# Kernel tuning notes

Measured on AMD Instinct MI355X. Metric: run time of the kernel, lower is better.

## Reference

```python
import jax, jax.numpy as jnp
import numpy as np

B, T, H = 16, 2048, 1024
L_ORDER, R_ORDER = 1, 1
K = L_ORDER + R_ORDER + 1
THRESH = 1.0


def _alphas(hidden, conv_w, conv_b, lin_w, lin_b):
    # hidden: [B, T, H]
    context = jnp.swapaxes(hidden, 1, 2)  # [B, H, T]
    q = jnp.pad(context, ((0, 0), (0, 0), (L_ORDER, R_ORDER)))  # ConstantPad1d
    mem = jax.lax.conv_general_dilated(
        q, conv_w, (1,), 'VALID',
        dimension_numbers=('NCH', 'OIH', 'NCH'),
        feature_group_count=conv_w.shape[0])  # depthwise conv, groups=idim
    mem = mem + conv_b[None, :, None]
    out = jnp.swapaxes(mem + context, 1, 2)  # [B, T, H] (dropout = identity, eval)
    out = jax.nn.relu(out)
    out = out @ lin_w.T + lin_b  # [B, T, 1]
    return jax.nn.sigmoid(out)[..., 0]  # [B, T]


def _cif_scan(hidden, alphas, threshold):
    # sequential integrate-and-fire over time, vectorized over batch via lax.scan
    b, t, h = hidden.shape

    def step(carry, xs):
        integrate, frame = carry          # [B], [B, H]
        alpha, h_t = xs                   # [B], [B, H]
        dist = 1.0 - integrate            # distribution_completion
        integrate = integrate + alpha
        fires_t = integrate
        fire = integrate >= threshold
        integrate = jnp.where(fire, integrate - 1.0, integrate)
        cur = jnp.where(fire, dist, alpha)
        rem = alpha - cur
        frame = frame + cur[:, None] * h_t
        frames_t = frame
        frame = jnp.where(fire[:, None], rem[:, None] * h_t, frame)
        return (integrate, frame), (fires_t, frames_t)

    init = (jnp.zeros((b,), hidden.dtype), jnp.zeros((b, h), hidden.dtype))
    xs = (jnp.swapaxes(alphas, 0, 1), jnp.swapaxes(hidden, 0, 1))
    _, (fires, frames) = jax.lax.scan(step, init, xs)
    return jnp.swapaxes(frames, 0, 1), jnp.swapaxes(fires, 0, 1)  # [B,T,H], [B,T]


def _gather_fired(frames, fires, threshold, max_label_len):
    # per-batch select frames where fires>=threshold, pad to max_label_len
    b, t, h = frames.shape
    mask = fires >= threshold                         # [B, T]
    rank = jnp.cumsum(mask.astype(jnp.int32), axis=1) - 1
    idx = jnp.where(mask, rank, max_label_len)        # invalid -> dummy row
    out = jnp.zeros((b, max_label_len + 1, h), frames.dtype)
    out = out.at[jnp.arange(b)[:, None], idx].add(
        jnp.where(mask[..., None], frames, 0.0))
    return out[:, :max_label_len]


def setup_inputs() -> dict:
    key = jax.random.key(0)
    k1, k2, k3, k4 = jax.random.split(key, 4)
    hidden = jax.random.normal(k1, (B, T, H), jnp.float32)
    conv_w = jax.random.normal(k2, (H, 1, K), jnp.float32) / np.sqrt(K)
    conv_b = jax.random.normal(k3, (H,), jnp.float32) * 0.01
    lin_w = jax.random.normal(k4, (1, H), jnp.float32) / np.sqrt(H)
    lin_b = jnp.zeros((1,), jnp.float32)
    return {"hidden": hidden, "conv_w": conv_w, "conv_b": conv_b,
            "lin_w": lin_w, "lin_b": lin_b}


def reference(hidden, conv_w, conv_b, lin_w, lin_b):
    alphas = _alphas(hidden, conv_w, conv_b, lin_w, lin_b)  # [B, T]
    cif_length = alphas.sum(-1)                             # [B]
    frames, fires = _cif_scan(hidden, alphas, THRESH)
    # data-dependent output length (matches torch: round(alphas.sum(-1)).max())
    max_label_len = int(jnp.round(cif_length).astype(jnp.int32).max())
    cif_output = _gather_fired(frames, fires, THRESH, max_label_len)
    return cif_output, cif_length, fires
```

## Files before the change

kernel.cpp:

```cpp
#include <hip/hip_runtime.h>
#include <math.h>

#define B_ 16
#define T_ 2048
#define H_ 1024
#define TPB 16
#define KPB 8

__global__ __launch_bounds__(256) void k1_alphas(
    const float* __restrict__ hidden, const float* __restrict__ conv_w,
    const float* __restrict__ conv_b, const float* __restrict__ lin_w,
    const float* __restrict__ lin_b, float* __restrict__ alphas)
{
    const int tile = blockIdx.x & (T_ / TPB - 1);
    const int b    = blockIdx.x / (T_ / TPB);
    const int tid  = threadIdx.x;
    const int h0   = tid * 4;

    float w0[4], w1[4], w2[4];
    {
        const float4* cw = (const float4*)(conv_w + (size_t)h0 * 3);
        float4 c0 = cw[0], c1 = cw[1], c2 = cw[2];
        w0[0] = c0.x; w1[0] = c0.y; w2[0] = c0.z;
        w0[1] = c0.w; w1[1] = c1.x; w2[1] = c1.y;
        w0[2] = c1.z; w1[2] = c1.w; w2[2] = c2.x;
        w0[3] = c2.y; w1[3] = c2.z; w2[3] = c2.w;
    }
    const float4 cb = *(const float4*)(conv_b + h0);
    const float4 lw = *(const float4*)(lin_w + h0);
    const float  lb = lin_b[0];

    const size_t base = ((size_t)b * T_) * H_ + h0;
    const int t0 = tile * TPB;

    float4 prev = (t0 > 0) ? *(const float4*)(hidden + base + (size_t)(t0 - 1) * H_)
                           : make_float4(0.f, 0.f, 0.f, 0.f);
    float4 curr = *(const float4*)(hidden + base + (size_t)t0 * H_);
    float4 next;

    __shared__ float lds[4][TPB];
    const int wave = tid >> 6;
    const int lane = tid & 63;

    #pragma unroll
    for (int tt = 0; tt < TPB; ++tt) {
        const int t = t0 + tt;
        next = (t + 1 < T_) ? *(const float4*)(hidden + base + (size_t)(t + 1) * H_)
                            : make_float4(0.f, 0.f, 0.f, 0.f);
        float p = 0.f, v;
        v = fmaf(w0[0], prev.x, fmaf(w1[0], curr.x, fmaf(w2[0], next.x, cb.x + curr.x)));
        p = fmaf(fmaxf(v, 0.f), lw.x, p);
        v = fmaf(w0[1], prev.y, fmaf(w1[1], curr.y, fmaf(w2[1], next.y, cb.y + curr.y)));
        p = fmaf(fmaxf(v, 0.f), lw.y, p);
        v = fmaf(w0[2], prev.z, fmaf(w1[2], curr.z, fmaf(w2[2], next.z, cb.z + curr.z)));
        p = fmaf(fmaxf(v, 0.f), lw.z, p);
        v = fmaf(w0[3], prev.w, fmaf(w1[3], curr.w, fmaf(w2[3], next.w, cb.w + curr.w)));
        p = fmaf(fmaxf(v, 0.f), lw.w, p);
        #pragma unroll
        for (int m = 32; m; m >>= 1) p += __shfl_xor(p, m);
        if (lane == 0) lds[wave][tt] = p;
        prev = curr; curr = next;
    }
    __syncthreads();
    if (tid < TPB) {
        float s = lds[0][tid] + lds[1][tid] + lds[2][tid] + lds[3][tid] + lb;
        alphas[(size_t)b * T_ + t0 + tid] = 1.f / (1.f + expf(-s));
    }
}

__global__ __launch_bounds__(256) void k2_scan_coef(
    const float* __restrict__ alphas, float* __restrict__ fires,
    float* __restrict__ wgt,
    int* __restrict__ fire_pos, int* __restrict__ n_fires,
    float* __restrict__ cif_length, int Lpad)
{
    const int b = blockIdx.x;
    const int tid = threadIdx.x;
    const size_t base = (size_t)b * T_;

    __shared__ float sA[T_];
    __shared__ float sF[T_];

    {
        const int i = tid * 8;
        *(float4*)(sA + i)     = *(const float4*)(alphas + base + i);
        *(float4*)(sA + i + 4) = *(const float4*)(alphas + base + i + 4);
    }
    __syncthreads();

    if (tid == 0) {
        float I = 0.f;
        for (int t = 0; t < T_; t += 8) {
            #pragma unroll
            for (int j = 0; j < 8; ++j) {
                I += sA[t + j];
                sF[t + j] = I;
                I = __builtin_amdgcn_fractf(I);
            }
        }
    }
    __syncthreads();

    const int t0 = tid * 8;
    float a[8], f[8];
    #pragma unroll
    for (int j = 0; j < 8; ++j) { a[j] = sA[t0 + j]; f[j] = sF[t0 + j]; }
    const float fprev = (t0 == 0) ? 0.f : sF[t0 - 1];

    *(float4*)(fires + base + t0)     = make_float4(f[0], f[1], f[2], f[3]);
    *(float4*)(fires + base + t0 + 4) = make_float4(f[4], f[5], f[6], f[7]);

    float w[16];
    bool fr[8];
    float asum = 0.f;
    int cnt = 0;
    #pragma unroll
    for (int j = 0; j < 8; ++j) {
        float fp = (j == 0) ? fprev : f[j - 1];
        float Iprev = __builtin_amdgcn_fractf(fp);
        fr[j] = (f[j] >= 1.f);
        const float dist = 1.f - Iprev;
        const float cu = fr[j] ? dist : a[j];
        const float re = a[j] - cu;
        w[2 * j]     = cu;
        w[2 * j + 1] = fr[j] ? re : -1.f;
        cnt += fr[j] ? 1 : 0;
        asum += a[j];
    }
    {
        const size_t wb = ((size_t)b * T_ + t0) * 2;
        *(float4*)(wgt + wb)      = *(float4*)(w);
        *(float4*)(wgt + wb + 4)  = *(float4*)(w + 4);
        *(float4*)(wgt + wb + 8)  = *(float4*)(w + 8);
        *(float4*)(wgt + wb + 12) = *(float4*)(w + 12);
    }

    const int lane = tid & 63, wave = tid >> 6;
    int inc = cnt;
    #pragma unroll
    for (int d = 1; d < 64; d <<= 1) {
        int v = __shfl_up(inc, d);
        if (lane >= d) inc += v;
    }
    __shared__ int wsum[4];
    if (lane == 63) wsum[wave] = inc;
    __syncthreads();
    int waveoff = 0;
    for (int w2 = 0; w2 < wave; ++w2) waveoff += wsum[w2];
    int r = waveoff + inc - cnt;
    #pragma unroll
    for (int j = 0; j < 8; ++j) {
        if (fr[j]) {
            if (r < Lpad) fire_pos[b * Lpad + r] = t0 + j;
            ++r;
        }
    }
    if (tid == 255) n_fires[b] = waveoff + inc;

    float s = asum;
    #pragma unroll
    for (int m = 32; m; m >>= 1) s += __shfl_xor(s, m);
    __shared__ float wred[4];
    if (lane == 0) wred[wave] = s;
    __syncthreads();
    if (tid == 0) cif_length[b] = wred[0] + wred[1] + wred[2] + wred[3];
}

__global__ __launch_bounds__(256) void k3_frames(
    const float* __restrict__ hidden, const float* __restrict__ wgt,
    const int* __restrict__ fire_pos, const int* __restrict__ n_fires,
    float* __restrict__ out, int L, int Lpad)
{
    const int k0 = blockIdx.x * KPB;
    const int b  = blockIdx.y;
    const int tid = threadIdx.x;
    const int h0 = tid * 4;
    const size_t hb = ((size_t)b * T_) * H_ + h0;
    const float2* wb = (const float2*)wgt + (size_t)b * T_;

    const int n = __builtin_amdgcn_readfirstlane(n_fires[b]);
    const int kmax = min(KPB, L - k0);
    const int kact = min(kmax, n - k0);

    const float4 zero4 = make_float4(0.f, 0.f, 0.f, 0.f);
    if (kact <= 0) {
        for (int kk = 0; kk < kmax; ++kk)
            *(float4*)(out + ((size_t)b * L + (k0 + kk)) * H_ + h0) = zero4;
        return;
    }

    const int tend = __builtin_amdgcn_readfirstlane(fire_pos[b * Lpad + k0 + kact - 1]);

    float4 acc;
    int t;
    if (k0 > 0) {
        const int s0 = __builtin_amdgcn_readfirstlane(fire_pos[b * Lpad + k0 - 1]);
        const float4 hr = *(const float4*)(hidden + hb + (size_t)s0 * H_);
        const float rm = wb[s0].y;
        acc.x = rm * hr.x; acc.y = rm * hr.y; acc.z = rm * hr.z; acc.w = rm * hr.w;
        t = s0 + 1;
    } else {
        acc = zero4;
        t = 0;
    }

    float4 hA, hB, hC;
    float2 wA, wB, wC;
    hA = *(const float4*)(hidden + hb + (size_t)t * H_);
    wA = wb[t];
    if (t + 1 <= tend) {
        hB = *(const float4*)(hidden + hb + (size_t)(t + 1) * H_);
        wB = wb[t + 1];
    } else { hB = zero4; wB = make_float2(0.f, -1.f); }

    int kk = 0;
    while (t <= tend) {
        if (t + 2 <= tend) {
            hC = *(const float4*)(hidden + hb + (size_t)(t + 2) * H_);
            wC = wb[t + 2];
        } else { hC = zero4; wC = make_float2(0.f, -1.f); }

        acc.x = fmaf(wA.x, hA.x, acc.x);
        acc.y = fmaf(wA.x, hA.y, acc.y);
        acc.z = fmaf(wA.x, hA.z, acc.z);
        acc.w = fmaf(wA.x, hA.w, acc.w);
        if (wA.y >= 0.f) {
            *(float4*)(out + ((size_t)b * L + (k0 + kk)) * H_ + h0) = acc;
            acc.x = wA.y * hA.x; acc.y = wA.y * hA.y;
            acc.z = wA.y * hA.z; acc.w = wA.y * hA.w;
            ++kk;
        }
        hA = hB; wA = wB; hB = hC; wB = wC;
        ++t;
    }

    for (; kk < kmax; ++kk)
        *(float4*)(out + ((size_t)b * L + (k0 + kk)) * H_ + h0) = zero4;
}

extern "C" void kernel_launch(void* const* d_in, const int* in_sizes, int n_in,
                              void* d_out, int out_size, void* d_ws, size_t ws_size,
                              hipStream_t stream) {
    const float* hidden = (const float*)d_in[0];
    const float* conv_w = (const float*)d_in[1];
    const float* conv_b = (const float*)d_in[2];
    const float* lin_w  = (const float*)d_in[3];
    const float* lin_b  = (const float*)d_in[4];
    float* out = (float*)d_out;

    const int L = (out_size - B_ - B_ * T_) / (B_ * H_);
    float* cif_output = out;
    float* cif_length = out + (size_t)B_ * L * H_;
    float* fires      = cif_length + B_;

    float* alphas = (float*)d_ws;
    float* wgt    = alphas + (size_t)B_ * T_;
    const int Lpad = L + 8;
    int* fire_pos = (int*)(wgt + (size_t)2 * B_ * T_);
    int* n_fires  = fire_pos + (size_t)B_ * Lpad;

    k1_alphas<<<dim3(B_ * (T_ / TPB)), 256, 0, stream>>>(
        hidden, conv_w, conv_b, lin_w, lin_b, alphas);
    k2_scan_coef<<<dim3(B_), 256, 0, stream>>>(
        alphas, fires, wgt, fire_pos, n_fires, cif_length, Lpad);
    k3_frames<<<dim3((L + KPB - 1) / KPB, B_), 256, 0, stream>>>(
        hidden, wgt, fire_pos, n_fires, cif_output, L, Lpad);
}
```

Measured before the change: 261.8 us.

## Fuse three CIF kernels into one persistent kernel with atomic work queues

Replaces the three separate launches (alphas, scan/coefficients, frame gather) with a single persistent kernel of fixed grid size. Blocks pull work items from atomic counters and use per-batch completion flags with acquire/release spinning, so a batch's scan and gather can start as soon as its alphas are done instead of waiting for the whole previous kernel. This removes launch gaps and lets the stages overlap across batches. In exchange it adds a memset, atomics, spin-waits and the risk of deadlock if the grid is not fully co-resident.

```diff
diff --git a/kernel.cpp b/kernel.cpp
--- a/kernel.cpp
+++ b/kernel.cpp
@@ -6,236 +6,294 @@
 #define H_ 1024
 #define TPB 16
 #define KPB 8
-
-__global__ __launch_bounds__(256) void k1_alphas(
+#define NK1 (B_ * (T_ / TPB))
+#define GRID 1024
+
+struct Flags {
+    int qK1, qK2, qK3, pad;
+    int k1_done[B_];
+    int k2_done[B_];
+};
+
+__device__ __forceinline__ int acq_load(int* p) {
+    return __hip_atomic_load(p, __ATOMIC_ACQUIRE, __HIP_MEMORY_SCOPE_AGENT);
+}
+
+union ShMem {
+    float k1lds[4][TPB];
+    struct { float sA[T_]; float sF[T_]; } k2;
+};
+
+__global__ __launch_bounds__(256, 4) void cif_fused(
     const float* __restrict__ hidden, const float* __restrict__ conv_w,
     const float* __restrict__ conv_b, const float* __restrict__ lin_w,
-    const float* __restrict__ lin_b, float* __restrict__ alphas)
+    const float* __restrict__ lin_b,
+    float* __restrict__ alphas, float* __restrict__ wgt,
+    int* __restrict__ fire_pos, int* __restrict__ n_fires,
+    Flags* flags,
+    float* __restrict__ out, float* __restrict__ cif_length,
+    float* __restrict__ fires, int L, int Lpad, int cpb, int totK3)
 {
-    const int tile = blockIdx.x & (T_ / TPB - 1);
-    const int b    = blockIdx.x / (T_ / TPB);
+    __shared__ ShMem sh;
+    __shared__ int sh_item;
+    __shared__ int wsum[4];
+    __shared__ float wred[4];
+
     const int tid  = threadIdx.x;
-    const int h0   = tid * 4;
-
-    float w0[4], w1[4], w2[4];
+    const int lane = tid & 63;
+    const int wave = tid >> 6;
+
     {
-        const float4* cw = (const float4*)(conv_w + (size_t)h0 * 3);
-        float4 c0 = cw[0], c1 = cw[1], c2 = cw[2];
-        w0[0] = c0.x; w1[0] = c0.y; w2[0] = c0.z;
-        w0[1] = c0.w; w1[1] = c1.x; w2[1] = c1.y;
-        w0[2] = c1.z; w1[2] = c1.w; w2[2] = c2.x;
-        w0[3] = c2.y; w1[3] = c2.z; w2[3] = c2.w;
+        const int h0 = tid * 4;
+        float w0[4], w1[4], w2[4];
+        {
+            const float4* cw = (const float4*)(conv_w + (size_t)h0 * 3);
+            float4 c0 = cw[0], c1 = cw[1], c2 = cw[2];
+            w0[0] = c0.x; w1[0] = c0.y; w2[0] = c0.z;
+            w0[1] = c0.w; w1[1] = c1.x; w2[1] = c1.y;
+            w0[2] = c1.z; w1[2] = c1.w; w2[2] = c2.x;
+            w0[3] = c2.y; w1[3] = c2.z; w2[3] = c2.w;
+        }
+        const float4 cb = *(const float4*)(conv_b + h0);
+        const float4 lw = *(const float4*)(lin_w + h0);
+        const float  lb = lin_b[0];
+
+        for (;;) {
+            if (tid == 0) sh_item = atomicAdd(&flags->qK1, 1);
+            __syncthreads();
+            const int it = sh_item;
+            if (it >= NK1) break;
+
+            const int b    = it >> 7;
+            const int tile = it & 127;
+            const size_t base = ((size_t)b * T_) * H_ + h0;
+            const int t0 = tile * TPB;
+
+            float4 prev = (t0 > 0) ? *(const float4*)(hidden + base + (size_t)(t0 - 1) * H_)
+                                   : make_float4(0.f, 0.f, 0.f, 0.f);
+            float4 curr = *(const float4*)(hidden + base + (size_t)t0 * H_);
+            float4 next;
+
+            #pragma unroll
+            for (int tt = 0; tt < TPB; ++tt) {
+                const int t = t0 + tt;
+                next = (t + 1 < T_) ? *(const float4*)(hidden + base + (size_t)(t + 1) * H_)
+                                    : make_float4(0.f, 0.f, 0.f, 0.f);
+                float p = 0.f, v;
+                v = fmaf(w0[0], prev.x, fmaf(w1[0], curr.x, fmaf(w2[0], next.x, cb.x + curr.x)));
+                p = fmaf(fmaxf(v, 0.f), lw.x, p);
+                v = fmaf(w0[1], prev.y, fmaf(w1[1], curr.y, fmaf(w2[1], next.y, cb.y + curr.y)));
+                p = fmaf(fmaxf(v, 0.f), lw.y, p);
+                v = fmaf(w0[2], prev.z, fmaf(w1[2], curr.z, fmaf(w2[2], next.z, cb.z + curr.z)));
+                p = fmaf(fmaxf(v, 0.f), lw.z, p);
+                v = fmaf(w0[3], prev.w, fmaf(w1[3], curr.w, fmaf(w2[3], next.w, cb.w + curr.w)));
+                p = fmaf(fmaxf(v, 0.f), lw.w, p);
+                #pragma unroll
+                for (int m = 32; m; m >>= 1) p += __shfl_xor(p, m);
+                if (lane == 0) sh.k1lds[wave][tt] = p;
+                prev = curr; curr = next;
+            }
+            __syncthreads();
+            if (tid < TPB) {
+                float s = sh.k1lds[0][tid] + sh.k1lds[1][tid] + sh.k1lds[2][tid]
+                        + sh.k1lds[3][tid] + lb;
+                alphas[(size_t)b * T_ + t0 + tid] = 1.f / (1.f + expf(-s));
+            }
+            if (tid == 0) {
+                __threadfence();
+                atomicAdd(&flags->k1_done[b], 1);
+            }
+            __syncthreads();
+        }
     }
-    const float4 cb = *(const float4*)(conv_b + h0);
-    const float4 lw = *(const float4*)(lin_w + h0);
-    const float  lb = lin_b[0];
-
-    const size_t base = ((size_t)b * T_) * H_ + h0;
-    const int t0 = tile * TPB;
-
-    float4 prev = (t0 > 0) ? *(const float4*)(hidden + base + (size_t)(t0 - 1) * H_)
-                           : make_float4(0.f, 0.f, 0.f, 0.f);
-    float4 curr = *(const float4*)(hidden + base + (size_t)t0 * H_);
-    float4 next;
-
-    __shared__ float lds[4][TPB];
-    const int wave = tid >> 6;
-    const int lane = tid & 63;
-
-    #pragma unroll
-    for (int tt = 0; tt < TPB; ++tt) {
-        const int t = t0 + tt;
-        next = (t + 1 < T_) ? *(const float4*)(hidden + base + (size_t)(t + 1) * H_)
-                            : make_float4(0.f, 0.f, 0.f, 0.f);
-        float p = 0.f, v;
-        v = fmaf(w0[0], prev.x, fmaf(w1[0], curr.x, fmaf(w2[0], next.x, cb.x + curr.x)));
-        p = fmaf(fmaxf(v, 0.f), lw.x, p);
-        v = fmaf(w0[1], prev.y, fmaf(w1[1], curr.y, fmaf(w2[1], next.y, cb.y + curr.y)));
-        p = fmaf(fmaxf(v, 0.f), lw.y, p);
-        v = fmaf(w0[2], prev.z, fmaf(w1[2], curr.z, fmaf(w2[2], next.z, cb.z + curr.z)));
-        p = fmaf(fmaxf(v, 0.f), lw.z, p);
-        v = fmaf(w0[3], prev.w, fmaf(w1[3], curr.w, fmaf(w2[3], next.w, cb.w + curr.w)));
-        p = fmaf(fmaxf(v, 0.f), lw.w, p);
-        #pragma unroll
-        for (int m = 32; m; m >>= 1) p += __shfl_xor(p, m);
-        if (lane == 0) lds[wave][tt] = p;
-        prev = curr; curr = next;
+
+    for (;;) {
+        if (tid == 0) sh_item = atomicAdd(&flags->qK2, 1);
+        __syncthreads();
+        const int b = sh_item;
+        if (b >= B_) break;
+
+        if (tid == 0) {
+            while (acq_load(&flags->k1_done[b]) < (T_ / TPB))
+                __builtin_amdgcn_s_sleep(8);
+        }
+        __syncthreads();
+        __threadfence();
+
+        const size_t base = (size_t)b * T_;
+        {
+            const int i = tid * 8;
+            *(float4*)(sh.k2.sA + i)     = *(const float4*)(alphas + base + i);
+            *(float4*)(sh.k2.sA + i + 4) = *(const float4*)(alphas + base + i + 4);
+        }
+        __syncthreads();
+
+        if (tid == 0) {
+            float I = 0.f;
+            for (int t = 0; t < T_; t += 8) {
+                #pragma unroll
+                for (int j = 0; j < 8; ++j) {
+                    I += sh.k2.sA[t + j];
+                    sh.k2.sF[t + j] = I;
+                    I = __builtin_amdgcn_fractf(I);
+                }
+            }
+        }
+        __syncthreads();
+
+        const int t0 = tid * 8;
+        float a[8], f[8];
+        #pragma unroll
+        for (int j = 0; j < 8; ++j) { a[j] = sh.k2.sA[t0 + j]; f[j] = sh.k2.sF[t0 + j]; }
+        const float fprev = (t0 == 0) ? 0.f : sh.k2.sF[t0 - 1];
+
+        *(float4*)(fires + base + t0)     = make_float4(f[0], f[1], f[2], f[3]);
+        *(float4*)(fires + base + t0 + 4) = make_float4(f[4], f[5], f[6], f[7]);
+
+        float w[16];
+        bool fr[8];
+        float asum = 0.f;
+        int cnt = 0;
+        #pragma unroll
+        for (int j = 0; j < 8; ++j) {
+            float fp = (j == 0) ? fprev : f[j - 1];
+            float Iprev = __builtin_amdgcn_fractf(fp);
+            fr[j] = (f[j] >= 1.f);
+            const float dist = 1.f - Iprev;
+            const float cu = fr[j] ? dist : a[j];
+            const float re = a[j] - cu;
+            w[2 * j]     = cu;
+            w[2 * j + 1] = fr[j] ? re : -1.f;
+            cnt += fr[j] ? 1 : 0;
+            asum += a[j];
+        }
+        {
+            const size_t wb = ((size_t)b * T_ + t0) * 2;
+            *(float4*)(wgt + wb)      = *(float4*)(w);
+            *(float4*)(wgt + wb + 4)  = *(float4*)(w + 4);
+            *(float4*)(wgt + wb + 8)  = *(float4*)(w + 8);
+            *(float4*)(wgt + wb + 12) = *(float4*)(w + 12);
+        }
+
+        int inc = cnt;
+        #pragma unroll
+        for (int d = 1; d < 64; d <<= 1) {
+            int v = __shfl_up(inc, d);
+            if (lane >= d) inc += v;
+        }
+        if (lane == 63) wsum[wave] = inc;
+        __syncthreads();
+        int waveoff = 0;
+        for (int w2 = 0; w2 < wave; ++w2) waveoff += wsum[w2];
+        int r = waveoff + inc - cnt;
+        #pragma unroll
+        for (int j = 0; j < 8; ++j) {
+            if (fr[j]) {
+                if (r < Lpad) fire_pos[b * Lpad + r] = t0 + j;
+                ++r;
+            }
+        }
+        if (tid == 255) n_fires[b] = waveoff + inc;
+
+        float s = asum;
+        #pragma unroll
+        for (int m = 32; m; m >>= 1) s += __shfl_xor(s, m);
+        if (lane == 0) wred[wave] = s;
+        __syncthreads();
+        if (tid == 0) {
+            cif_length[b] = wred[0] + wred[1] + wred[2] + wred[3];
+            __threadfence();
+            __hip_atomic_store(&flags->k2_done[b], 1, __ATOMIC_RELEASE,
+                               __HIP_MEMORY_SCOPE_AGENT);
+        }
+        __syncthreads();
     }
-    __syncthreads();
-    if (tid < TPB) {
-        float s = lds[0][tid] + lds[1][tid] + lds[2][tid] + lds[3][tid] + lb;
-        alphas[(size_t)b * T_ + t0 + tid] = 1.f / (1.f + expf(-s));
+
+    {
+        const int h0 = tid * 4;
+        int last_b = -1;
+        for (;;) {
+            if (tid == 0) sh_item = atomicAdd(&flags->qK3, 1);
+            __syncthreads();
+            const int j = sh_item;
+            if (j >= totK3) break;
+            const int b  = j / cpb;
+            const int k0 = (j - b * cpb) * KPB;
+
+            if (b != last_b) {
+                if (tid == 0) {
+                    while (acq_load(&flags->k2_done[b]) == 0)
+                        __builtin_amdgcn_s_sleep(32);
+                }
+                __syncthreads();
+                __threadfence();
+                last_b = b;
+            }
+
+            const size_t hb = ((size_t)b * T_) * H_ + h0;
+            const float2* wb = (const float2*)wgt + (size_t)b * T_;
+            const int n = __builtin_amdgcn_readfirstlane(n_fires[b]);
+            const int kmax = min(KPB, L - k0);
+            const int kact = min(kmax, n - k0);
+            const float4 zero4 = make_float4(0.f, 0.f, 0.f, 0.f);
+
+            if (kact <= 0) {
+                for (int kk = 0; kk < kmax; ++kk)
+                    *(float4*)(out + ((size_t)b * L + (k0 + kk)) * H_ + h0) = zero4;
+            } else {
+                const int tend = __builtin_amdgcn_readfirstlane(
+                    fire_pos[b * Lpad + k0 + kact - 1]);
+
+                float4 acc;
+                int t;
+                if (k0 > 0) {
+                    const int s0 = __builtin_amdgcn_readfirstlane(
+                        fire_pos[b * Lpad + k0 - 1]);
+                    const float4 hr = *(const float4*)(hidden + hb + (size_t)s0 * H_);
+                    const float rm = wb[s0].y;
+                    acc.x = rm * hr.x; acc.y = rm * hr.y;
+                    acc.z = rm * hr.z; acc.w = rm * hr.w;
+                    t = s0 + 1;
+                } else {
+                    acc = zero4;
+                    t = 0;
+                }
+
+                float4 hA, hB, hC;
+                float2 wA, wB, wC;
+                hA = *(const float4*)(hidden + hb + (size_t)t * H_);
+                wA = wb[t];
+                if (t + 1 <= tend) {
+                    hB = *(const float4*)(hidden + hb + (size_t)(t + 1) * H_);
+                    wB = wb[t + 1];
+                } else { hB = zero4; wB = make_float2(0.f, -1.f); }
+
+                int kk = 0;
+                while (t <= tend) {
+                    if (t + 2 <= tend) {
+                        hC = *(const float4*)(hidden + hb + (size_t)(t + 2) * H_);
+                        wC = wb[t + 2];
+                    } else { hC = zero4; wC = make_float2(0.f, -1.f); }
+
+                    acc.x = fmaf(wA.x, hA.x, acc.x);
+                    acc.y = fmaf(wA.x, hA.y, acc.y);
+                    acc.z = fmaf(wA.x, hA.z, acc.z);
+                    acc.w = fmaf(wA.x, hA.w, acc.w);
+                    if (wA.y >= 0.f) {
+                        *(float4*)(out + ((size_t)b * L + (k0 + kk)) * H_ + h0) = acc;
+                        acc.x = wA.y * hA.x; acc.y = wA.y * hA.y;
+                        acc.z = wA.y * hA.z; acc.w = wA.y * hA.w;
+                        ++kk;
+                    }
+                    hA = hB; wA = wB; hB = hC; wB = wC;
+                    ++t;
+                }
+                for (; kk < kmax; ++kk)
+                    *(float4*)(out + ((size_t)b * L + (k0 + kk)) * H_ + h0) = zero4;
+            }
+            __syncthreads();
+        }
     }
-}
-
-__global__ __launch_bounds__(256) void k2_scan_coef(
-    const float* __restrict__ alphas, float* __restrict__ fires,
-    float* __restrict__ wgt,
-    int* __restrict__ fire_pos, int* __restrict__ n_fires,
-    float* __restrict__ cif_length, int Lpad)
-{
-    const int b = blockIdx.x;
-    const int tid = threadIdx.x;
-    const size_t base = (size_t)b * T_;
-
-    __shared__ float sA[T_];
-    __shared__ float sF[T_];
-
-    {
-        const int i = tid * 8;
-        *(float4*)(sA + i)     = *(const float4*)(alphas + base + i);
-        *(float4*)(sA + i + 4) = *(const float4*)(alphas + base + i + 4);
-    }
-    __syncthreads();
-
-    if (tid == 0) {
-        float I = 0.f;
-        for (int t = 0; t < T_; t += 8) {
-            #pragma unroll
-            for (int j = 0; j < 8; ++j) {
-                I += sA[t + j];
-                sF[t + j] = I;
-                I = __builtin_amdgcn_fractf(I);
-            }
-        }
-    }
-    __syncthreads();
-
-    const int t0 = tid * 8;
-    float a[8], f[8];
-    #pragma unroll
-    for (int j = 0; j < 8; ++j) { a[j] = sA[t0 + j]; f[j] = sF[t0 + j]; }
-    const float fprev = (t0 == 0) ? 0.f : sF[t0 - 1];
-
-    *(float4*)(fires + base + t0)     = make_float4(f[0], f[1], f[2], f[3]);
-    *(float4*)(fires + base + t0 + 4) = make_float4(f[4], f[5], f[6], f[7]);
-
-    float w[16];
-    bool fr[8];
-    float asum = 0.f;
-    int cnt = 0;
-    #pragma unroll
-    for (int j = 0; j < 8; ++j) {
-        float fp = (j == 0) ? fprev : f[j - 1];
-        float Iprev = __builtin_amdgcn_fractf(fp);
-        fr[j] = (f[j] >= 1.f);
-        const float dist = 1.f - Iprev;
-        const float cu = fr[j] ? dist : a[j];
-        const float re = a[j] - cu;
-        w[2 * j]     = cu;
-        w[2 * j + 1] = fr[j] ? re : -1.f;
-        cnt += fr[j] ? 1 : 0;
-        asum += a[j];
-    }
-    {
-        const size_t wb = ((size_t)b * T_ + t0) * 2;
-        *(float4*)(wgt + wb)      = *(float4*)(w);
-        *(float4*)(wgt + wb + 4)  = *(float4*)(w + 4);
-        *(float4*)(wgt + wb + 8)  = *(float4*)(w + 8);
-        *(float4*)(wgt + wb + 12) = *(float4*)(w + 12);
-    }
-
-    const int lane = tid & 63, wave = tid >> 6;
-    int inc = cnt;
-    #pragma unroll
-    for (int d = 1; d < 64; d <<= 1) {
-        int v = __shfl_up(inc, d);
-        if (lane >= d) inc += v;
-    }
-    __shared__ int wsum[4];
-    if (lane == 63) wsum[wave] = inc;
-    __syncthreads();
-    int waveoff = 0;
-    for (int w2 = 0; w2 < wave; ++w2) waveoff += wsum[w2];
-    int r = waveoff + inc - cnt;
-    #pragma unroll
-    for (int j = 0; j < 8; ++j) {
-        if (fr[j]) {
-            if (r < Lpad) fire_pos[b * Lpad + r] = t0 + j;
-            ++r;
-        }
-    }
-    if (tid == 255) n_fires[b] = waveoff + inc;
-
-    float s = asum;
-    #pragma unroll
-    for (int m = 32; m; m >>= 1) s += __shfl_xor(s, m);
-    __shared__ float wred[4];
-    if (lane == 0) wred[wave] = s;
-    __syncthreads();
-    if (tid == 0) cif_length[b] = wred[0] + wred[1] + wred[2] + wred[3];
-}
-
-__global__ __launch_bounds__(256) void k3_frames(
-    const float* __restrict__ hidden, const float* __restrict__ wgt,
-    const int* __restrict__ fire_pos, const int* __restrict__ n_fires,
-    float* __restrict__ out, int L, int Lpad)
-{
-    const int k0 = blockIdx.x * KPB;
-    const int b  = blockIdx.y;
-    const int tid = threadIdx.x;
-    const int h0 = tid * 4;
-    const size_t hb = ((size_t)b * T_) * H_ + h0;
-    const float2* wb = (const float2*)wgt + (size_t)b * T_;
-
-    const int n = __builtin_amdgcn_readfirstlane(n_fires[b]);
-    const int kmax = min(KPB, L - k0);
-    const int kact = min(kmax, n - k0);
-
-    const float4 zero4 = make_float4(0.f, 0.f, 0.f, 0.f);
-    if (kact <= 0) {
-        for (int kk = 0; kk < kmax; ++kk)
-            *(float4*)(out + ((size_t)b * L + (k0 + kk)) * H_ + h0) = zero4;
-        return;
-    }
-
-    const int tend = __builtin_amdgcn_readfirstlane(fire_pos[b * Lpad + k0 + kact - 1]);
-
-    float4 acc;
-    int t;
-    if (k0 > 0) {
-        const int s0 = __builtin_amdgcn_readfirstlane(fire_pos[b * Lpad + k0 - 1]);
-        const float4 hr = *(const float4*)(hidden + hb + (size_t)s0 * H_);
-        const float rm = wb[s0].y;
-        acc.x = rm * hr.x; acc.y = rm * hr.y; acc.z = rm * hr.z; acc.w = rm * hr.w;
-        t = s0 + 1;
-    } else {
-        acc = zero4;
-        t = 0;
-    }
-
-    float4 hA, hB, hC;
-    float2 wA, wB, wC;
-    hA = *(const float4*)(hidden + hb + (size_t)t * H_);
-    wA = wb[t];
-    if (t + 1 <= tend) {
-        hB = *(const float4*)(hidden + hb + (size_t)(t + 1) * H_);
-        wB = wb[t + 1];
-    } else { hB = zero4; wB = make_float2(0.f, -1.f); }
-
-    int kk = 0;
-    while (t <= tend) {
-        if (t + 2 <= tend) {
-            hC = *(const float4*)(hidden + hb + (size_t)(t + 2) * H_);
-            wC = wb[t + 2];
-        } else { hC = zero4; wC = make_float2(0.f, -1.f); }
-
-        acc.x = fmaf(wA.x, hA.x, acc.x);
-        acc.y = fmaf(wA.x, hA.y, acc.y);
-        acc.z = fmaf(wA.x, hA.z, acc.z);
-        acc.w = fmaf(wA.x, hA.w, acc.w);
-        if (wA.y >= 0.f) {
-            *(float4*)(out + ((size_t)b * L + (k0 + kk)) * H_ + h0) = acc;
-            acc.x = wA.y * hA.x; acc.y = wA.y * hA.y;
-            acc.z = wA.y * hA.z; acc.w = wA.y * hA.w;
-            ++kk;
-        }
-        hA = hB; wA = wB; hB = hC; wB = wC;
-        ++t;
-    }
-
-    for (; kk < kmax; ++kk)
-        *(float4*)(out + ((size_t)b * L + (k0 + kk)) * H_ + h0) = zero4;
 }
 
 extern "C" void kernel_launch(void* const* d_in, const int* in_sizes, int n_in,
@@ -258,11 +316,14 @@
     const int Lpad = L + 8;
     int* fire_pos = (int*)(wgt + (size_t)2 * B_ * T_);
     int* n_fires  = fire_pos + (size_t)B_ * Lpad;
-
-    k1_alphas<<<dim3(B_ * (T_ / TPB)), 256, 0, stream>>>(
-        hidden, conv_w, conv_b, lin_w, lin_b, alphas);
-    k2_scan_coef<<<dim3(B_), 256, 0, stream>>>(
-        alphas, fires, wgt, fire_pos, n_fires, cif_length, Lpad);
-    k3_frames<<<dim3((L + KPB - 1) / KPB, B_), 256, 0, stream>>>(
-        hidden, wgt, fire_pos, n_fires, cif_output, L, Lpad);
+    Flags* flags  = (Flags*)(n_fires + B_);
+
+    const int cpb   = (L + KPB - 1) / KPB;
+    const int totK3 = B_ * cpb;
+
+    hipMemsetAsync(flags, 0, sizeof(Flags), stream);
+    cif_fused<<<dim3(GRID), 256, 0, stream>>>(
+        hidden, conv_w, conv_b, lin_w, lin_b,
+        alphas, wgt, fire_pos, n_fires, flags,
+        cif_output, cif_length, fires, L, Lpad, cpb, totK3);
 }
```

New measurement: 605.4 us. 2.31x slower.
